# Kernel tuning notes

Measured on AMD Instinct MI355X. Metric: run time of the kernel, lower is better.

## Reference

```python
import jax, jax.numpy as jnp
import numpy as np

TAU = 0.5          # proto_tau
TOPK = 3           # slot_topk
BETA = 0.5         # soft-topk temperature
BETA_SUP = 0.4     # support_beta
T_SUP = 1.6        # support_tsup
KAPPA_FEAT = 1.0   # support_kappa_feat
CMAX = 64          # num classes


def setup_inputs() -> dict:
    key = jax.random.key(0)
    k0, k1, k2, k3 = jax.random.split(key, 4)
    B, M, D, K = 128, 64, 512, 4096
    feats_bmd = jax.random.normal(k0, (B, M, D), jnp.float32)
    slot_prob = jax.random.uniform(k1, (B, M), jnp.float32)
    slot_mask = jnp.ones((M,), jnp.float32)
    S_slots = jax.random.normal(k2, (B, M, D), jnp.float32)
    C = jax.random.normal(k3, (K, D), jnp.float32)
    # every class gets K//CMAX prototypes (torch.unique loop covers all classes)
    C_cls = jnp.arange(K, dtype=jnp.int32) % CMAX
    alpha = jnp.array(1.0, jnp.float32)
    return dict(feats_bmd=feats_bmd, slot_prob=slot_prob, slot_mask=slot_mask,
                S_slots=S_slots, C=C, C_cls=C_cls, alpha=alpha)


def _l2norm(x, eps=1e-12):
    return x / jnp.maximum(jnp.linalg.norm(x, axis=-1, keepdims=True), eps)


def _soft_topk_weights(p, mask, k=TOPK, beta=BETA):
    # p: (B,M), mask: (1,M)
    p = p * mask
    _, topi = jax.lax.top_k(p, k)                          # (B,k)
    keep = jnp.zeros_like(p).at[jnp.arange(p.shape[0])[:, None], topi].set(1.0)
    q = p * keep
    z = (q - q.mean(axis=1, keepdims=True)) / beta
    w = jax.nn.softmax(z, axis=1) * mask
    return w / jnp.maximum(w.sum(axis=1, keepdims=True), 1e-8)


def _class_lse(sim, cls, num_classes, tau=TAU):
    # segmented logsumexp over prototypes grouped by class id (replaces the
    # per-class masked_fill loop in the original).
    B, M, K = sim.shape
    s = sim.reshape(B * M, K).T                                   # (K, BM)
    xmax = jax.ops.segment_max(s, cls, num_segments=num_classes)  # (C, BM)
    e = jnp.exp((s - xmax[cls]) / tau)
    ssum = jax.ops.segment_sum(e, cls, num_segments=num_classes)  # (C, BM)
    evi = xmax + tau * jnp.log(jnp.maximum(ssum, 1e-8))
    return evi.T.reshape(B, M, num_classes)


def _top1_plus_support(evi, P, S_slots):
    # evi: (B,M,C), P: (B,M), S_slots: (B,M,D)
    B, M, C = evi.shape
    score = evi * P[:, :, None]
    top1_idx = jnp.argmax(score, axis=1)                    # (B,C)
    top1_val = jnp.max(score, axis=1)                       # (B,C)
    P_sup = jax.nn.softmax(jnp.log(P + 1e-8) / T_SUP, axis=1)  # (B,M)
    S = _l2norm(S_slots)
    top1_feat = jnp.take_along_axis(S, top1_idx[:, :, None], axis=1)  # (B,C,D)
    cos = jnp.maximum(jnp.einsum('bmd,bcd->bmc', S, top1_feat), 0.0)
    w_red = KAPPA_FEAT * cos
    support_raw = evi + jnp.log(jnp.maximum(P_sup, 1e-8))[:, :, None] - w_red
    is_top1 = jnp.arange(M)[None, :, None] == top1_idx[:, None, :]    # (B,M,C)
    support_raw = jnp.where(is_top1, -10000.0, support_raw)
    support_val = jax.nn.logsumexp(support_raw, axis=1)
    return top1_val + BETA_SUP * support_val


def reference(feats_bmd, slot_prob, slot_mask, S_slots, C, C_cls, alpha):
    w = _soft_topk_weights(slot_prob, slot_mask[None, :])
    f = _l2norm(feats_bmd)
    sim = jnp.einsum('bmd,kd->bmk', f, C)        # (B,M,K) similarity GEMM
    evi_all = _class_lse(sim, C_cls, CMAX)       # (B,M,Cmax)
    proto_logits = _top1_plus_support(evi_all, w, S_slots)
    return alpha * proto_logits                  # (B, Cmax)
```

## Files before the change

### kernel.cpp

```cpp
#include <hip/hip_runtime.h>
#include <stdint.h>


typedef short   short8_t  __attribute__((ext_vector_type(8)));
typedef unsigned short ushort8_t __attribute__((ext_vector_type(8)));
typedef float   floatx4   __attribute__((ext_vector_type(4)));

#define B_N   128
#define M_N   64
#define D_N   512
#define K_N   4096
#define ROWS  8192

__device__ __forceinline__ unsigned short f2bf(float f){
  unsigned u = __float_as_uint(f);
  u = (u + 0x7FFFu + ((u >> 16) & 1u)) >> 16;
  return (unsigned short)u;
}
__device__ __forceinline__ float bf2f(unsigned short s){
  return __uint_as_float(((unsigned)s) << 16);
}

__global__ void k_weights(const float* __restrict__ prob, const float* __restrict__ mask,
                          float* __restrict__ w_out, float* __restrict__ lps_out){
  const int b = blockIdx.x, m = threadIdx.x;
  const float mk = mask[m];
  float p = prob[b*M_N + m] * mk;

  float pw = p, keep = 0.f;
  for(int it = 0; it < 3; ++it){
    float v = pw; int idx = m;
    #pragma unroll
    for(int off = 32; off > 0; off >>= 1){
      float ov = __shfl_xor(v, off);
      int   oi = __shfl_xor(idx, off);
      if(ov > v || (ov == v && oi < idx)){ v = ov; idx = oi; }
    }
    if(m == idx){ keep = 1.f; pw = -1e30f; }
  }
  float q = p * keep;
  float s = q;
  #pragma unroll
  for(int off = 32; off > 0; off >>= 1) s += __shfl_xor(s, off);
  float z = (q - s * (1.f/64.f)) * 2.0f;
  float zm = z;
  #pragma unroll
  for(int off = 32; off > 0; off >>= 1) zm = fmaxf(zm, __shfl_xor(zm, off));
  float e = expf(z - zm);
  float es = e;
  #pragma unroll
  for(int off = 32; off > 0; off >>= 1) es += __shfl_xor(es, off);
  float wv = (e / es) * mk;
  float ws = wv;
  #pragma unroll
  for(int off = 32; off > 0; off >>= 1) ws += __shfl_xor(ws, off);
  wv = wv / fmaxf(ws, 1e-8f);
  w_out[b*M_N + m] = wv;

  float l = logf(wv + 1e-8f) * (1.0f/1.6f);
  float lm = l;
  #pragma unroll
  for(int off = 32; off > 0; off >>= 1) lm = fmaxf(lm, __shfl_xor(lm, off));
  float ee = expf(l - lm);
  float ees = ee;
  #pragma unroll
  for(int off = 32; off > 0; off >>= 1) ees += __shfl_xor(ees, off);
  float psup = ee / ees;
  lps_out[b*M_N + m] = logf(fmaxf(psup, 1e-8f));
}

__global__ void k_prep(const float* __restrict__ src, unsigned short* __restrict__ hi,
                       unsigned short* __restrict__ lo, float* __restrict__ f32o, int mode){
  const int lane = threadIdx.x & 63;
  const int row  = blockIdx.x * 4 + (threadIdx.x >> 6);
  const float4* r = (const float4*)(src + (size_t)row * D_N);
  float4 a = r[lane*2], c = r[lane*2 + 1];
  float inv = 1.f;
  if(mode < 2){
    float ss = a.x*a.x + a.y*a.y + a.z*a.z + a.w*a.w
             + c.x*c.x + c.y*c.y + c.z*c.z + c.w*c.w;
    #pragma unroll
    for(int off = 32; off > 0; off >>= 1) ss += __shfl_xor(ss, off);
    inv = 1.f / fmaxf(sqrtf(ss), 1e-12f);
  }
  float v[8] = {a.x*inv, a.y*inv, a.z*inv, a.w*inv, c.x*inv, c.y*inv, c.z*inv, c.w*inv};
  if(mode == 1){
    float4* o = (float4*)(f32o + (size_t)row * D_N);
    o[lane*2]     = make_float4(v[0], v[1], v[2], v[3]);
    o[lane*2 + 1] = make_float4(v[4], v[5], v[6], v[7]);
  } else {
    ushort8_t h, L;
    #pragma unroll
    for(int i = 0; i < 8; ++i){
      h[i] = f2bf(v[i]);
      L[i] = f2bf(v[i] - bf2f(h[i]));
    }
    ((ushort8_t*)(hi + (size_t)row * D_N))[lane] = h;
    ((ushort8_t*)(lo + (size_t)row * D_N))[lane] = L;
  }
}

__device__ __forceinline__ floatx4 mfma16(short8_t a, short8_t b, floatx4 c){
  return __builtin_amdgcn_mfma_f32_16x16x32_bf16(a, b, c, 0, 0, 0);
}

__global__ __launch_bounds__(512, 2) void k_gemm_lse(
    const unsigned short* __restrict__ fhi, const unsigned short* __restrict__ flo,
    const unsigned short* __restrict__ chi, const unsigned short* __restrict__ clo,
    float* __restrict__ part){
  __shared__ char smem[81920];
  const int bid = blockIdx.x;
  const int kh  = bid & 1;
  const int rg  = bid >> 1;
  const int tid = threadIdx.x;
  const int w = tid >> 6, lane = tid & 63;
  const int wr = w >> 2, wc = w & 3;
  const int l15 = lane & 15, l4 = lane >> 4, ax = l15 & 7;

  const int arow = tid >> 3, as = tid & 7;
  const int aoff = arow*128 + ((as ^ (arow & 7)) << 4);
  const char* aph = (const char*)fhi + (size_t)(rg*64 + arow)*1024 + as*16;
  const char* apl = (const char*)flo + (size_t)(rg*64 + arow)*1024 + as*16;
  const char* bph = (const char*)chi + (size_t)(kh*2048 + arow)*1024 + as*16;
  const char* bpl = (const char*)clo + (size_t)(kh*2048 + arow)*1024 + as*16;

  const int arB = (32*wr + l15) * 128;
  const int brB = (wc*16 + l15) * 128;

  const floatx4 vzero = {0.f, 0.f, 0.f, 0.f};
  floatx4 cacc[2];
  cacc[0] = vzero; cacc[1] = vzero;

  for(int t0 = 0; t0 < 8; ++t0){
    floatx4 sim[2][4];
    #pragma unroll
    for(int rt = 0; rt < 2; ++rt){
      #pragma unroll
      for(int kt = 0; kt < 4; ++kt){ sim[rt][kt] = vzero; }
    }
    const size_t koff = (size_t)t0 * 262144;

    for(int dc = 0; dc < 8; ++dc){
      const size_t doff = (size_t)dc * 128;
      __syncthreads();
      short8_t va = *(const short8_t*)(aph + doff);
      short8_t vl = *(const short8_t*)(apl + doff);
      short8_t b0 = *(const short8_t*)(bph + koff + doff);
      short8_t b1 = *(const short8_t*)(bph + koff + 65536  + doff);
      short8_t b2 = *(const short8_t*)(bph + koff + 131072 + doff);
      short8_t b3 = *(const short8_t*)(bph + koff + 196608 + doff);
      short8_t c0 = *(const short8_t*)(bpl + koff + doff);
      short8_t c1 = *(const short8_t*)(bpl + koff + 65536  + doff);
      short8_t c2 = *(const short8_t*)(bpl + koff + 131072 + doff);
      short8_t c3 = *(const short8_t*)(bpl + koff + 196608 + doff);
      *(short8_t*)(smem + aoff)                 = va;
      *(short8_t*)(smem + 8192  + aoff)         = vl;
      *(short8_t*)(smem + 16384 + aoff)         = b0;
      *(short8_t*)(smem + 16384 + 8192  + aoff) = b1;
      *(short8_t*)(smem + 16384 + 16384 + aoff) = b2;
      *(short8_t*)(smem + 16384 + 24576 + aoff) = b3;
      *(short8_t*)(smem + 49152 + aoff)         = c0;
      *(short8_t*)(smem + 49152 + 8192  + aoff) = c1;
      *(short8_t*)(smem + 49152 + 16384 + aoff) = c2;
      *(short8_t*)(smem + 49152 + 24576 + aoff) = c3;
      __syncthreads();

      #pragma unroll
      for(int ks = 0; ks < 2; ++ks){
        const int sx = ((ks*4 + l4) ^ ax) << 4;
        short8_t ah0 = *(const short8_t*)(smem + arB + sx);
        short8_t ah1 = *(const short8_t*)(smem + arB + 2048 + sx);
        short8_t al0 = *(const short8_t*)(smem + 8192 + arB + sx);
        short8_t al1 = *(const short8_t*)(smem + 8192 + arB + 2048 + sx);
        short8_t bh[4], bl[4];
        #pragma unroll
        for(int kt = 0; kt < 4; ++kt){
          bh[kt] = *(const short8_t*)(smem + 16384 + kt*8192 + brB + sx);
          bl[kt] = *(const short8_t*)(smem + 49152 + kt*8192 + brB + sx);
        }
        #pragma unroll
        for(int kt = 0; kt < 4; ++kt){
          sim[0][kt] = mfma16(ah0, bh[kt], sim[0][kt]);
          sim[0][kt] = mfma16(al0, bh[kt], sim[0][kt]);
          sim[0][kt] = mfma16(ah0, bl[kt], sim[0][kt]);
          sim[1][kt] = mfma16(ah1, bh[kt], sim[1][kt]);
          sim[1][kt] = mfma16(al1, bh[kt], sim[1][kt]);
          sim[1][kt] = mfma16(ah1, bl[kt], sim[1][kt]);
        }
      }
    }
    #pragma unroll
    for(int rt = 0; rt < 2; ++rt){
      #pragma unroll
      for(int kt = 0; kt < 4; ++kt){
        #pragma unroll
        for(int e = 0; e < 4; ++e){
          cacc[rt][e] += __expf(2.0f * sim[rt][kt][e]);
        }
      }
    }
  }

  #pragma unroll
  for(int rt = 0; rt < 2; ++rt){
    #pragma unroll
    for(int e = 0; e < 4; ++e){
      const int r = 32*wr + 16*rt + l4*4 + e;
      part[((size_t)kh*ROWS + rg*64 + r)*64 + wc*16 + l15] = cacc[rt][e];
    }
  }
}

#define SPAD 516
__global__ __launch_bounds__(256) void k_epi(
    const float* __restrict__ part, const float* __restrict__ Snorm,
    const float* __restrict__ w_in, const float* __restrict__ lps_in,
    const float* __restrict__ alpha_p, float* __restrict__ out){
  __shared__ float Ss[64 * SPAD];
  __shared__ float evi[64 * 64];
  __shared__ float w_s[64], lps_s[64], t1v[64];
  __shared__ int   t1i[64];
  __shared__ float red[16 * 64];
  const int b = blockIdx.x, tid = threadIdx.x;

  if(tid < 64){ w_s[tid] = w_in[b*64 + tid]; lps_s[tid] = lps_in[b*64 + tid]; }
  for(int i = tid; i < 4096; i += 256){
    float s0 = part[(size_t)b*4096 + i];
    float s1 = part[(size_t)524288 + (size_t)b*4096 + i];
    evi[i] = 0.5f * logf(s0 + s1);
  }
  const float4* sg = (const float4*)(Snorm + (size_t)b * 32768);
  for(int i = tid; i < 8192; i += 256){
    int r = i >> 7, c4 = i & 127;
    *(float4*)&Ss[r*SPAD + c4*4] = sg[i];
  }
  __syncthreads();

  if(tid < 64){
    float bv = -1e30f; int bi = 0;
    for(int m = 0; m < 64; ++m){
      float sc = evi[m*64 + tid] * w_s[m];
      if(sc > bv){ bv = sc; bi = m; }
    }
    t1v[tid] = bv; t1i[tid] = bi;
  }
  __syncthreads();

  const int mi = tid >> 4, ci = tid & 15;
  float acc[4][4];
  #pragma unroll
  for(int i = 0; i < 4; ++i){
    #pragma unroll
    for(int j = 0; j < 4; ++j){ acc[i][j] = 0.f; }
  }
  int tr[4];
  #pragma unroll
  for(int q = 0; q < 4; ++q) tr[q] = t1i[ci*4 + q];

  for(int d4 = 0; d4 < 128; ++d4){
    float4 sv[4], tv[4];
    #pragma unroll
    for(int q = 0; q < 4; ++q) sv[q] = *(const float4*)&Ss[(mi*4 + q)*SPAD + d4*4];
    #pragma unroll
    for(int q = 0; q < 4; ++q) tv[q] = *(const float4*)&Ss[tr[q]*SPAD + d4*4];
    #pragma unroll
    for(int i = 0; i < 4; ++i){
      #pragma unroll
      for(int j = 0; j < 4; ++j){
        acc[i][j] += sv[i].x*tv[j].x + sv[i].y*tv[j].y + sv[i].z*tv[j].z + sv[i].w*tv[j].w;
      }
    }
  }

  float ps[4] = {0.f, 0.f, 0.f, 0.f};
  #pragma unroll
  for(int i = 0; i < 4; ++i){
    const int m = mi*4 + i;
    #pragma unroll
    for(int q = 0; q < 4; ++q){
      const int c = ci*4 + q;
      float sr = evi[m*64 + c] + lps_s[m] - fmaxf(acc[i][q], 0.f);
      ps[q] += (m == tr[q]) ? 0.f : expf(sr);
    }
  }
  #pragma unroll
  for(int q = 0; q < 4; ++q) red[mi*64 + ci*4 + q] = ps[q];
  __syncthreads();

  if(tid < 64){
    float s = 0.f;
    for(int i = 0; i < 16; ++i) s += red[i*64 + tid];
    out[b*64 + tid] = alpha_p[0] * (t1v[tid] + 0.4f * logf(s));
  }
}

extern "C" void kernel_launch(void* const* d_in, const int* in_sizes, int n_in,
                              void* d_out, int out_size, void* d_ws, size_t ws_size,
                              hipStream_t stream){
  const float* feats     = (const float*)d_in[0];
  const float* slot_prob = (const float*)d_in[1];
  const float* slot_mask = (const float*)d_in[2];
  const float* S_slots   = (const float*)d_in[3];
  const float* Cmat      = (const float*)d_in[4];
  const float* alpha     = (const float*)d_in[6];

  char* ws = (char*)d_ws;
  unsigned short* fhi = (unsigned short*)(ws);
  unsigned short* flo = (unsigned short*)(ws + (8  << 20));
  unsigned short* chi = (unsigned short*)(ws + (16 << 20));
  unsigned short* clo = (unsigned short*)(ws + (20 << 20));
  float* part  = (float*)(ws + (24 << 20));
  float* wbuf  = (float*)(ws + (28 << 20));
  float* lps   = (float*)(ws + (28 << 20) + 32768);
  float* Snorm = (float*)(ws + (28 << 20) + 65536);
  float* outp  = (float*)d_out;

  k_weights<<<dim3(128), dim3(64), 0, stream>>>(slot_prob, slot_mask, wbuf, lps);
  k_prep<<<dim3(2048), dim3(256), 0, stream>>>(feats,   fhi, flo, nullptr, 0);
  k_prep<<<dim3(2048), dim3(256), 0, stream>>>(S_slots, nullptr, nullptr, Snorm, 1);
  k_prep<<<dim3(1024), dim3(256), 0, stream>>>(Cmat,    chi, clo, nullptr, 2);
  k_gemm_lse<<<dim3(256), dim3(512), 0, stream>>>(fhi, flo, chi, clo, part);
  k_epi<<<dim3(128), dim3(256), 0, stream>>>(part, Snorm, wbuf, lps, alpha, outp);
}
```

Baseline: 261.9 us.

## Prefetch GEMM tiles, split K four ways, fuse prep and weight kernels

The GEMM-LSE kernel now prefetches the next global tile into registers while the MFMAs run on the current shared-memory tile, and raises MFMA priority with s_setprio. The K dimension is split four ways across 512 blocks instead of two ways across 256. Small kernels are merged: the weights computation and the S_slots normalization move into the epilogue, and the feats and C prep run as one launch. This removes launch overhead and the Snorm round-trip through global memory. The cost is higher register pressure, more partial sums to combine, and more work in the epilogue.

```diff
diff --git a/kernel.cpp b/kernel.cpp
--- a/kernel.cpp
+++ b/kernel.cpp
@@ -21,62 +21,19 @@
   return __uint_as_float(((unsigned)s) << 16);
 }
 
-__global__ void k_weights(const float* __restrict__ prob, const float* __restrict__ mask,
-                          float* __restrict__ w_out, float* __restrict__ lps_out){
-  const int b = blockIdx.x, m = threadIdx.x;
-  const float mk = mask[m];
-  float p = prob[b*M_N + m] * mk;
-
-  float pw = p, keep = 0.f;
-  for(int it = 0; it < 3; ++it){
-    float v = pw; int idx = m;
-    #pragma unroll
-    for(int off = 32; off > 0; off >>= 1){
-      float ov = __shfl_xor(v, off);
-      int   oi = __shfl_xor(idx, off);
-      if(ov > v || (ov == v && oi < idx)){ v = ov; idx = oi; }
-    }
-    if(m == idx){ keep = 1.f; pw = -1e30f; }
-  }
-  float q = p * keep;
-  float s = q;
-  #pragma unroll
-  for(int off = 32; off > 0; off >>= 1) s += __shfl_xor(s, off);
-  float z = (q - s * (1.f/64.f)) * 2.0f;
-  float zm = z;
-  #pragma unroll
-  for(int off = 32; off > 0; off >>= 1) zm = fmaxf(zm, __shfl_xor(zm, off));
-  float e = expf(z - zm);
-  float es = e;
-  #pragma unroll
-  for(int off = 32; off > 0; off >>= 1) es += __shfl_xor(es, off);
-  float wv = (e / es) * mk;
-  float ws = wv;
-  #pragma unroll
-  for(int off = 32; off > 0; off >>= 1) ws += __shfl_xor(ws, off);
-  wv = wv / fmaxf(ws, 1e-8f);
-  w_out[b*M_N + m] = wv;
-
-  float l = logf(wv + 1e-8f) * (1.0f/1.6f);
-  float lm = l;
-  #pragma unroll
-  for(int off = 32; off > 0; off >>= 1) lm = fmaxf(lm, __shfl_xor(lm, off));
-  float ee = expf(l - lm);
-  float ees = ee;
-  #pragma unroll
-  for(int off = 32; off > 0; off >>= 1) ees += __shfl_xor(ees, off);
-  float psup = ee / ees;
-  lps_out[b*M_N + m] = logf(fmaxf(psup, 1e-8f));
-}
-
-__global__ void k_prep(const float* __restrict__ src, unsigned short* __restrict__ hi,
-                       unsigned short* __restrict__ lo, float* __restrict__ f32o, int mode){
+__global__ __launch_bounds__(256) void k_prep(
+    const float* __restrict__ feats, const float* __restrict__ Cm,
+    unsigned short* __restrict__ fhi, unsigned short* __restrict__ flo,
+    unsigned short* __restrict__ chi, unsigned short* __restrict__ clo){
+  const int bid = blockIdx.x;
+  const bool isF = bid < 2048;
   const int lane = threadIdx.x & 63;
-  const int row  = blockIdx.x * 4 + (threadIdx.x >> 6);
+  const int row  = (isF ? bid : bid - 2048) * 4 + (threadIdx.x >> 6);
+  const float* src = isF ? feats : Cm;
   const float4* r = (const float4*)(src + (size_t)row * D_N);
   float4 a = r[lane*2], c = r[lane*2 + 1];
   float inv = 1.f;
-  if(mode < 2){
+  if(isF){
     float ss = a.x*a.x + a.y*a.y + a.z*a.z + a.w*a.w
              + c.x*c.x + c.y*c.y + c.z*c.z + c.w*c.w;
     #pragma unroll
@@ -84,45 +41,41 @@
     inv = 1.f / fmaxf(sqrtf(ss), 1e-12f);
   }
   float v[8] = {a.x*inv, a.y*inv, a.z*inv, a.w*inv, c.x*inv, c.y*inv, c.z*inv, c.w*inv};
-  if(mode == 1){
-    float4* o = (float4*)(f32o + (size_t)row * D_N);
-    o[lane*2]     = make_float4(v[0], v[1], v[2], v[3]);
-    o[lane*2 + 1] = make_float4(v[4], v[5], v[6], v[7]);
-  } else {
-    ushort8_t h, L;
-    #pragma unroll
-    for(int i = 0; i < 8; ++i){
-      h[i] = f2bf(v[i]);
-      L[i] = f2bf(v[i] - bf2f(h[i]));
-    }
-    ((ushort8_t*)(hi + (size_t)row * D_N))[lane] = h;
-    ((ushort8_t*)(lo + (size_t)row * D_N))[lane] = L;
-  }
+  ushort8_t h, L;
+  #pragma unroll
+  for(int i = 0; i < 8; ++i){
+    h[i] = f2bf(v[i]);
+    L[i] = f2bf(v[i] - bf2f(h[i]));
+  }
+  unsigned short* hi = isF ? fhi : chi;
+  unsigned short* lo = isF ? flo : clo;
+  ((ushort8_t*)(hi + (size_t)row * D_N))[lane] = h;
+  ((ushort8_t*)(lo + (size_t)row * D_N))[lane] = L;
 }
 
 __device__ __forceinline__ floatx4 mfma16(short8_t a, short8_t b, floatx4 c){
   return __builtin_amdgcn_mfma_f32_16x16x32_bf16(a, b, c, 0, 0, 0);
 }
 
-__global__ __launch_bounds__(512, 2) void k_gemm_lse(
+__global__ __launch_bounds__(512, 4) void k_gemm_lse(
     const unsigned short* __restrict__ fhi, const unsigned short* __restrict__ flo,
     const unsigned short* __restrict__ chi, const unsigned short* __restrict__ clo,
     float* __restrict__ part){
   __shared__ char smem[81920];
   const int bid = blockIdx.x;
-  const int kh  = bid & 1;
-  const int rg  = bid >> 1;
+  const int kq  = bid & 3;
+  const int rg  = bid >> 2;
   const int tid = threadIdx.x;
   const int w = tid >> 6, lane = tid & 63;
   const int wr = w >> 2, wc = w & 3;
   const int l15 = lane & 15, l4 = lane >> 4, ax = l15 & 7;
 
-  const int arow = tid >> 3, as = tid & 7;
-  const int aoff = arow*128 + ((as ^ (arow & 7)) << 4);
-  const char* aph = (const char*)fhi + (size_t)(rg*64 + arow)*1024 + as*16;
-  const char* apl = (const char*)flo + (size_t)(rg*64 + arow)*1024 + as*16;
-  const char* bph = (const char*)chi + (size_t)(kh*2048 + arow)*1024 + as*16;
-  const char* bpl = (const char*)clo + (size_t)(kh*2048 + arow)*1024 + as*16;
+  const int srow = tid >> 3, ss = tid & 7;
+  const int aoff = srow*128 + ((ss ^ (srow & 7)) << 4);
+  const char* aH = (const char*)fhi + (size_t)(rg*64 + srow)*1024 + ss*16;
+  const char* aL = (const char*)flo + (size_t)(rg*64 + srow)*1024 + ss*16;
+  const char* bH = (const char*)chi + (size_t)(kq*1024 + srow)*1024 + ss*16;
+  const char* bL = (const char*)clo + (size_t)(kq*1024 + srow)*1024 + ss*16;
 
   const int arB = (32*wr + l15) * 128;
   const int brB = (wc*16 + l15) * 128;
@@ -130,91 +83,105 @@
   const floatx4 vzero = {0.f, 0.f, 0.f, 0.f};
   floatx4 cacc[2];
   cacc[0] = vzero; cacc[1] = vzero;
-
-  for(int t0 = 0; t0 < 8; ++t0){
-    floatx4 sim[2][4];
-    #pragma unroll
-    for(int rt = 0; rt < 2; ++rt){
-      #pragma unroll
-      for(int kt = 0; kt < 4; ++kt){ sim[rt][kt] = vzero; }
-    }
-    const size_t koff = (size_t)t0 * 262144;
-
-    for(int dc = 0; dc < 8; ++dc){
-      const size_t doff = (size_t)dc * 128;
-      __syncthreads();
-      short8_t va = *(const short8_t*)(aph + doff);
-      short8_t vl = *(const short8_t*)(apl + doff);
-      short8_t b0 = *(const short8_t*)(bph + koff + doff);
-      short8_t b1 = *(const short8_t*)(bph + koff + 65536  + doff);
-      short8_t b2 = *(const short8_t*)(bph + koff + 131072 + doff);
-      short8_t b3 = *(const short8_t*)(bph + koff + 196608 + doff);
-      short8_t c0 = *(const short8_t*)(bpl + koff + doff);
-      short8_t c1 = *(const short8_t*)(bpl + koff + 65536  + doff);
-      short8_t c2 = *(const short8_t*)(bpl + koff + 131072 + doff);
-      short8_t c3 = *(const short8_t*)(bpl + koff + 196608 + doff);
-      *(short8_t*)(smem + aoff)                 = va;
-      *(short8_t*)(smem + 8192  + aoff)         = vl;
-      *(short8_t*)(smem + 16384 + aoff)         = b0;
-      *(short8_t*)(smem + 16384 + 8192  + aoff) = b1;
-      *(short8_t*)(smem + 16384 + 16384 + aoff) = b2;
-      *(short8_t*)(smem + 16384 + 24576 + aoff) = b3;
-      *(short8_t*)(smem + 49152 + aoff)         = c0;
-      *(short8_t*)(smem + 49152 + 8192  + aoff) = c1;
-      *(short8_t*)(smem + 49152 + 16384 + aoff) = c2;
-      *(short8_t*)(smem + 49152 + 24576 + aoff) = c3;
-      __syncthreads();
-
-      #pragma unroll
-      for(int ks = 0; ks < 2; ++ks){
-        const int sx = ((ks*4 + l4) ^ ax) << 4;
-        short8_t ah0 = *(const short8_t*)(smem + arB + sx);
-        short8_t ah1 = *(const short8_t*)(smem + arB + 2048 + sx);
-        short8_t al0 = *(const short8_t*)(smem + 8192 + arB + sx);
-        short8_t al1 = *(const short8_t*)(smem + 8192 + arB + 2048 + sx);
-        short8_t bh[4], bl[4];
+  floatx4 sim[2][4];
+  #pragma unroll
+  for(int rt = 0; rt < 2; ++rt)
+    #pragma unroll
+    for(int kt = 0; kt < 4; ++kt) sim[rt][kt] = vzero;
+
+  short8_t pre[10];
+  {
+    pre[0] = *(const short8_t*)(aH);
+    pre[1] = *(const short8_t*)(aL);
+    #pragma unroll
+    for(int kt = 0; kt < 4; ++kt) pre[2+kt] = *(const short8_t*)(bH + kt*65536);
+    #pragma unroll
+    for(int kt = 0; kt < 4; ++kt) pre[6+kt] = *(const short8_t*)(bL + kt*65536);
+    *(short8_t*)(smem + aoff)         = pre[0];
+    *(short8_t*)(smem + 8192  + aoff) = pre[1];
+    #pragma unroll
+    for(int kt = 0; kt < 4; ++kt) *(short8_t*)(smem + 16384 + kt*8192 + aoff) = pre[2+kt];
+    #pragma unroll
+    for(int kt = 0; kt < 4; ++kt) *(short8_t*)(smem + 49152 + kt*8192 + aoff) = pre[6+kt];
+  }
+  __syncthreads();
+
+  #pragma unroll 1
+  for(int s = 0; s < 32; ++s){
+    const int dc = s & 7;
+    if(s < 31){
+      const int sn = s + 1;
+      const int koff = (sn >> 3) * 262144;
+      const int doff = (sn & 7) * 128;
+      pre[0] = *(const short8_t*)(aH + doff);
+      pre[1] = *(const short8_t*)(aL + doff);
+      #pragma unroll
+      for(int kt = 0; kt < 4; ++kt)
+        pre[2+kt] = *(const short8_t*)(bH + koff + kt*65536 + doff);
+      #pragma unroll
+      for(int kt = 0; kt < 4; ++kt)
+        pre[6+kt] = *(const short8_t*)(bL + koff + kt*65536 + doff);
+    }
+
+    __builtin_amdgcn_s_setprio(1);
+    #pragma unroll
+    for(int ks = 0; ks < 2; ++ks){
+      const int sx = ((ks*4 + l4) ^ ax) << 4;
+      short8_t ah0 = *(const short8_t*)(smem + arB + sx);
+      short8_t ah1 = *(const short8_t*)(smem + arB + 2048 + sx);
+      short8_t al0 = *(const short8_t*)(smem + 8192 + arB + sx);
+      short8_t al1 = *(const short8_t*)(smem + 8192 + arB + 2048 + sx);
+      #pragma unroll
+      for(int kt = 0; kt < 4; ++kt){
+        short8_t bh = *(const short8_t*)(smem + 16384 + kt*8192 + brB + sx);
+        short8_t bl = *(const short8_t*)(smem + 49152 + kt*8192 + brB + sx);
+        sim[0][kt] = mfma16(ah0, bh, sim[0][kt]);
+        sim[0][kt] = mfma16(al0, bh, sim[0][kt]);
+        sim[0][kt] = mfma16(ah0, bl, sim[0][kt]);
+        sim[1][kt] = mfma16(ah1, bh, sim[1][kt]);
+        sim[1][kt] = mfma16(al1, bh, sim[1][kt]);
+        sim[1][kt] = mfma16(ah1, bl, sim[1][kt]);
+      }
+    }
+    __builtin_amdgcn_s_setprio(0);
+
+    if(dc == 7){
+      #pragma unroll
+      for(int rt = 0; rt < 2; ++rt)
         #pragma unroll
         for(int kt = 0; kt < 4; ++kt){
-          bh[kt] = *(const short8_t*)(smem + 16384 + kt*8192 + brB + sx);
-          bl[kt] = *(const short8_t*)(smem + 49152 + kt*8192 + brB + sx);
+          #pragma unroll
+          for(int e = 0; e < 4; ++e)
+            cacc[rt][e] += __expf(2.0f * sim[rt][kt][e]);
+          sim[rt][kt] = vzero;
         }
-        #pragma unroll
-        for(int kt = 0; kt < 4; ++kt){
-          sim[0][kt] = mfma16(ah0, bh[kt], sim[0][kt]);
-          sim[0][kt] = mfma16(al0, bh[kt], sim[0][kt]);
-          sim[0][kt] = mfma16(ah0, bl[kt], sim[0][kt]);
-          sim[1][kt] = mfma16(ah1, bh[kt], sim[1][kt]);
-          sim[1][kt] = mfma16(al1, bh[kt], sim[1][kt]);
-          sim[1][kt] = mfma16(ah1, bl[kt], sim[1][kt]);
-        }
-      }
-    }
-    #pragma unroll
-    for(int rt = 0; rt < 2; ++rt){
-      #pragma unroll
-      for(int kt = 0; kt < 4; ++kt){
-        #pragma unroll
-        for(int e = 0; e < 4; ++e){
-          cacc[rt][e] += __expf(2.0f * sim[rt][kt][e]);
-        }
-      }
-    }
-  }
-
-  #pragma unroll
-  for(int rt = 0; rt < 2; ++rt){
+    }
+
+    __syncthreads();
+    if(s < 31){
+      *(short8_t*)(smem + aoff)         = pre[0];
+      *(short8_t*)(smem + 8192  + aoff) = pre[1];
+      #pragma unroll
+      for(int kt = 0; kt < 4; ++kt) *(short8_t*)(smem + 16384 + kt*8192 + aoff) = pre[2+kt];
+      #pragma unroll
+      for(int kt = 0; kt < 4; ++kt) *(short8_t*)(smem + 49152 + kt*8192 + aoff) = pre[6+kt];
+      __syncthreads();
+    }
+  }
+
+  #pragma unroll
+  for(int rt = 0; rt < 2; ++rt)
     #pragma unroll
     for(int e = 0; e < 4; ++e){
       const int r = 32*wr + 16*rt + l4*4 + e;
-      part[((size_t)kh*ROWS + rg*64 + r)*64 + wc*16 + l15] = cacc[rt][e];
-    }
-  }
+      part[((size_t)kq*ROWS + rg*64 + r)*64 + wc*16 + l15] = cacc[rt][e];
+    }
 }
 
 #define SPAD 516
 __global__ __launch_bounds__(256) void k_epi(
-    const float* __restrict__ part, const float* __restrict__ Snorm,
-    const float* __restrict__ w_in, const float* __restrict__ lps_in,
+    const float* __restrict__ part, const float* __restrict__ S_raw,
+    const float* __restrict__ prob, const float* __restrict__ maskp,
     const float* __restrict__ alpha_p, float* __restrict__ out){
   __shared__ float Ss[64 * SPAD];
   __shared__ float evi[64 * 64];
@@ -223,16 +190,80 @@
   __shared__ float red[16 * 64];
   const int b = blockIdx.x, tid = threadIdx.x;
 
-  if(tid < 64){ w_s[tid] = w_in[b*64 + tid]; lps_s[tid] = lps_in[b*64 + tid]; }
+  if(tid < 64){
+    const int m = tid;
+    const float mk = maskp[m];
+    float p = prob[b*M_N + m] * mk;
+    float pw = p, keep = 0.f;
+    for(int it = 0; it < 3; ++it){
+      float v = pw; int idx = m;
+      #pragma unroll
+      for(int off = 32; off > 0; off >>= 1){
+        float ov = __shfl_xor(v, off);
+        int   oi = __shfl_xor(idx, off);
+        if(ov > v || (ov == v && oi < idx)){ v = ov; idx = oi; }
+      }
+      if(m == idx){ keep = 1.f; pw = -1e30f; }
+    }
+    float q = p * keep;
+    float s = q;
+    #pragma unroll
+    for(int off = 32; off > 0; off >>= 1) s += __shfl_xor(s, off);
+    float z = (q - s * (1.f/64.f)) * 2.0f;
+    float zm = z;
+    #pragma unroll
+    for(int off = 32; off > 0; off >>= 1) zm = fmaxf(zm, __shfl_xor(zm, off));
+    float e = expf(z - zm);
+    float es = e;
+    #pragma unroll
+    for(int off = 32; off > 0; off >>= 1) es += __shfl_xor(es, off);
+    float wv = (e / es) * mk;
+    float ws = wv;
+    #pragma unroll
+    for(int off = 32; off > 0; off >>= 1) ws += __shfl_xor(ws, off);
+    wv = wv / fmaxf(ws, 1e-8f);
+    w_s[m] = wv;
+    float l = logf(wv + 1e-8f) * (1.0f/1.6f);
+    float lm = l;
+    #pragma unroll
+    for(int off = 32; off > 0; off >>= 1) lm = fmaxf(lm, __shfl_xor(lm, off));
+    float ee = expf(l - lm);
+    float ees = ee;
+    #pragma unroll
+    for(int off = 32; off > 0; off >>= 1) ees += __shfl_xor(ees, off);
+    lps_s[m] = logf(fmaxf(ee / ees, 1e-8f));
+  }
+
   for(int i = tid; i < 4096; i += 256){
-    float s0 = part[(size_t)b*4096 + i];
-    float s1 = part[(size_t)524288 + (size_t)b*4096 + i];
-    evi[i] = 0.5f * logf(s0 + s1);
-  }
-  const float4* sg = (const float4*)(Snorm + (size_t)b * 32768);
+    float s = part[(size_t)b*4096 + i]
+            + part[(size_t)1*ROWS*64 + (size_t)b*4096 + i]
+            + part[(size_t)2*ROWS*64 + (size_t)b*4096 + i]
+            + part[(size_t)3*ROWS*64 + (size_t)b*4096 + i];
+    evi[i] = 0.5f * logf(s);
+  }
+  const float4* sg = (const float4*)(S_raw + (size_t)b * 32768);
   for(int i = tid; i < 8192; i += 256){
     int r = i >> 7, c4 = i & 127;
     *(float4*)&Ss[r*SPAD + c4*4] = sg[i];
+  }
+  __syncthreads();
+
+  {
+    const int lane = tid & 63;
+    for(int it = 0; it < 16; ++it){
+      const int row = it*4 + (tid >> 6);
+      float4 x = *(const float4*)&Ss[row*SPAD + lane*8];
+      float4 y = *(const float4*)&Ss[row*SPAD + lane*8 + 4];
+      float ss = x.x*x.x + x.y*x.y + x.z*x.z + x.w*x.w
+               + y.x*y.x + y.y*y.y + y.z*y.z + y.w*y.w;
+      #pragma unroll
+      for(int off = 32; off > 0; off >>= 1) ss += __shfl_xor(ss, off);
+      float inv = 1.f / fmaxf(sqrtf(ss), 1e-12f);
+      x.x*=inv; x.y*=inv; x.z*=inv; x.w*=inv;
+      y.x*=inv; y.y*=inv; y.z*=inv; y.w*=inv;
+      *(float4*)&Ss[row*SPAD + lane*8]     = x;
+      *(float4*)&Ss[row*SPAD + lane*8 + 4] = y;
+    }
   }
   __syncthreads();
 
@@ -249,10 +280,9 @@
   const int mi = tid >> 4, ci = tid & 15;
   float acc[4][4];
   #pragma unroll
-  for(int i = 0; i < 4; ++i){
-    #pragma unroll
-    for(int j = 0; j < 4; ++j){ acc[i][j] = 0.f; }
-  }
+  for(int i = 0; i < 4; ++i)
+    #pragma unroll
+    for(int j = 0; j < 4; ++j) acc[i][j] = 0.f;
   int tr[4];
   #pragma unroll
   for(int q = 0; q < 4; ++q) tr[q] = t1i[ci*4 + q];
@@ -264,12 +294,10 @@
     #pragma unroll
     for(int q = 0; q < 4; ++q) tv[q] = *(const float4*)&Ss[tr[q]*SPAD + d4*4];
     #pragma unroll
-    for(int i = 0; i < 4; ++i){
-      #pragma unroll
-      for(int j = 0; j < 4; ++j){
+    for(int i = 0; i < 4; ++i)
+      #pragma unroll
+      for(int j = 0; j < 4; ++j)
         acc[i][j] += sv[i].x*tv[j].x + sv[i].y*tv[j].y + sv[i].z*tv[j].z + sv[i].w*tv[j].w;
-      }
-    }
   }
 
   float ps[4] = {0.f, 0.f, 0.f, 0.f};
@@ -310,15 +338,10 @@
   unsigned short* chi = (unsigned short*)(ws + (16 << 20));
   unsigned short* clo = (unsigned short*)(ws + (20 << 20));
   float* part  = (float*)(ws + (24 << 20));
-  float* wbuf  = (float*)(ws + (28 << 20));
-  float* lps   = (float*)(ws + (28 << 20) + 32768);
-  float* Snorm = (float*)(ws + (28 << 20) + 65536);
   float* outp  = (float*)d_out;
 
-  k_weights<<<dim3(128), dim3(64), 0, stream>>>(slot_prob, slot_mask, wbuf, lps);
-  k_prep<<<dim3(2048), dim3(256), 0, stream>>>(feats,   fhi, flo, nullptr, 0);
-  k_prep<<<dim3(2048), dim3(256), 0, stream>>>(S_slots, nullptr, nullptr, Snorm, 1);
-  k_prep<<<dim3(1024), dim3(256), 0, stream>>>(Cmat,    chi, clo, nullptr, 2);
-  k_gemm_lse<<<dim3(256), dim3(512), 0, stream>>>(fhi, flo, chi, clo, part);
-  k_epi<<<dim3(128), dim3(256), 0, stream>>>(part, Snorm, wbuf, lps, alpha, outp);
-}
+  k_prep<<<dim3(3072), dim3(256), 0, stream>>>(feats, Cmat, fhi, flo, chi, clo);
+  k_gemm_lse<<<dim3(512), dim3(512), 0, stream>>>(fhi, flo, chi, clo, part);
+  k_epi<<<dim3(128), dim3(256), 0, stream>>>(part, S_slots, slot_prob, slot_mask,
+                                             alpha, outp);
+}
```

New measurement: 225.4 us. 13.9% less time.
